# Kernel tuning notes

Hardware: AMD Instinct MI355X
Metric: run time of the kernel (lower is better)

The kernel has to match this reference:

```python
import jax, jax.numpy as jnp
import numpy as np

N_NODES = 50000
N_EDGES = 800000
HIDDEN = 128
MLP_DIM = 64

def setup_inputs() -> dict:
    key = jax.random.key(0)
    k1, k2, k3, k4 = jax.random.split(key, 4)
    node_emb = jax.random.normal(k1, (N_NODES, HIDDEN), dtype=jnp.float32)
    edge_index = jax.random.randint(k2, (2, N_EDGES), 0, N_NODES, dtype=jnp.int64)
    # Xavier-uniform init like the torch module
    lim1 = float(np.sqrt(6.0 / (2 * HIDDEN + MLP_DIM)))
    lim2 = float(np.sqrt(6.0 / (MLP_DIM + 1)))
    W1 = jax.random.uniform(k3, (2 * HIDDEN, MLP_DIM), minval=-lim1, maxval=lim1, dtype=jnp.float32)
    b1 = jnp.zeros((MLP_DIM,), dtype=jnp.float32)
    W2 = jax.random.uniform(k4, (MLP_DIM, 1), minval=-lim2, maxval=lim2, dtype=jnp.float32)
    b2 = jnp.zeros((1,), dtype=jnp.float32)
    return {"node_emb": node_emb, "edge_index": edge_index, "W1": W1, "b1": b1, "W2": W2, "b2": b2}

def reference(node_emb, edge_index, W1, b1, W2, b2):
    src, dst = edge_index[0], edge_index[1]
    emb_src = node_emb[src]                      # [E, H] gather
    emb_dst = node_emb[dst]                      # [E, H] gather
    edge_emb = jnp.concatenate([emb_src, emb_dst], axis=1)  # [E, 2H]
    h = jax.nn.relu(edge_emb @ W1 + b1)          # [E, MLP_DIM]
    edge_logits = h @ W2 + b2                    # [E, 1]
    return edge_logits
```

## Files before the change

kernel.cpp:

```cpp
#include <hip/hip_runtime.h>


#define HIDDEN 128

typedef __attribute__((ext_vector_type(8))) short bf16x8;
typedef __attribute__((ext_vector_type(4))) float f32x4;
typedef __attribute__((ext_vector_type(8))) _Float16 half8;

__device__ inline unsigned short f32_to_bf16(float f) {
    unsigned int u = __float_as_uint(f);
    unsigned int r = (u + 0x7fffu + ((u >> 16) & 1u)) >> 16;
    return (unsigned short)r;
}

__global__ __launch_bounds__(256) void precompute_pq_mfma(
    const float* __restrict__ node_emb,
    const float* __restrict__ W1,
    _Float16* __restrict__ PQ,
    int n_nodes)
{
    __shared__ unsigned short As[128 * 136];
    __shared__ unsigned short Bt[128 * 136];

    const int t = threadIdx.x;
    const int m0 = blockIdx.x * 128;

    #pragma unroll 4
    for (int s = 0; s < 16; ++s) {
        int slot = s * 256 + t;
        int row = slot >> 5;
        int k0 = (slot & 31) * 4;
        int m = m0 + row;
        float4 v = make_float4(0.f, 0.f, 0.f, 0.f);
        if (m < n_nodes) v = *(const float4*)&node_emb[(size_t)m * 128 + k0];
        ushort4 w;
        w.x = f32_to_bf16(v.x); w.y = f32_to_bf16(v.y);
        w.z = f32_to_bf16(v.z); w.w = f32_to_bf16(v.w);
        *(ushort4*)&As[row * 136 + k0] = w;
    }
    for (int u = t; u < 256 * 64; u += 256) {
        int r = u >> 6;
        int c = u & 63;
        int j = (r < 128) ? c : (c + 64);
        int k = r & 127;
        Bt[j * 136 + k] = f32_to_bf16(W1[u]);
    }
    __syncthreads();

    const int wave = t >> 6;
    const int lane = t & 63;
    const int lrow = lane & 15;
    const int kq = (lane >> 4) * 8;

    f32x4 acc[2][8];
    #pragma unroll
    for (int rs = 0; rs < 2; ++rs)
        #pragma unroll
        for (int c = 0; c < 8; ++c)
            acc[rs][c] = (f32x4){0.f, 0.f, 0.f, 0.f};

    #pragma unroll
    for (int k0 = 0; k0 < 128; k0 += 32) {
        bf16x8 a[2];
        #pragma unroll
        for (int rs = 0; rs < 2; ++rs)
            a[rs] = *(const bf16x8*)&As[(wave * 32 + rs * 16 + lrow) * 136 + k0 + kq];
        #pragma unroll
        for (int c = 0; c < 8; ++c) {
            bf16x8 b = *(const bf16x8*)&Bt[(c * 16 + lrow) * 136 + k0 + kq];
            acc[0][c] = __builtin_amdgcn_mfma_f32_16x16x32_bf16(a[0], b, acc[0][c], 0, 0, 0);
            acc[1][c] = __builtin_amdgcn_mfma_f32_16x16x32_bf16(a[1], b, acc[1][c], 0, 0, 0);
        }
    }

    const int rbase = (lane >> 4) * 4;
    #pragma unroll
    for (int rs = 0; rs < 2; ++rs) {
        #pragma unroll
        for (int reg = 0; reg < 4; ++reg) {
            int m = m0 + wave * 32 + rs * 16 + rbase + reg;
            if (m < n_nodes) {
                #pragma unroll
                for (int c = 0; c < 8; ++c) {
                    int col = c * 16 + lrow;
                    PQ[(size_t)m * 128 + col] = (_Float16)acc[rs][c][reg];
                }
            }
        }
    }
}

__global__ __launch_bounds__(256) void edge_mlp16(
    const _Float16* __restrict__ PQ,
    const int* __restrict__ edge_index,
    const float* __restrict__ b1,
    const float* __restrict__ W2,
    const float* __restrict__ b2,
    float* __restrict__ out,
    int E)
{
    const int t = threadIdx.x;
    const int g = t & 7;
    const int e = blockIdx.x * 32 + (t >> 3);
    if (e >= E) return;

    const int src = edge_index[e];
    const int dst = edge_index[E + e];

    half8 p = *(const half8*)&PQ[(size_t)src * 128 + g * 8];
    half8 q = *(const half8*)&PQ[(size_t)dst * 128 + 64 + g * 8];
    float4 bA = *(const float4*)&b1[g * 8];
    float4 bB = *(const float4*)&b1[g * 8 + 4];
    float4 wA = *(const float4*)&W2[g * 8];
    float4 wB = *(const float4*)&W2[g * 8 + 4];

    float partial = 0.f;
    partial += fmaxf((float)p[0] + (float)q[0] + bA.x, 0.f) * wA.x;
    partial += fmaxf((float)p[1] + (float)q[1] + bA.y, 0.f) * wA.y;
    partial += fmaxf((float)p[2] + (float)q[2] + bA.z, 0.f) * wA.z;
    partial += fmaxf((float)p[3] + (float)q[3] + bA.w, 0.f) * wA.w;
    partial += fmaxf((float)p[4] + (float)q[4] + bB.x, 0.f) * wB.x;
    partial += fmaxf((float)p[5] + (float)q[5] + bB.y, 0.f) * wB.y;
    partial += fmaxf((float)p[6] + (float)q[6] + bB.z, 0.f) * wB.z;
    partial += fmaxf((float)p[7] + (float)q[7] + bB.w, 0.f) * wB.w;

    partial += __shfl_xor(partial, 1, 64);
    partial += __shfl_xor(partial, 2, 64);
    partial += __shfl_xor(partial, 4, 64);

    if (g == 0) out[e] = partial + b2[0];
}

extern "C" void kernel_launch(void* const* d_in, const int* in_sizes, int n_in,
                              void* d_out, int out_size, void* d_ws, size_t ws_size,
                              hipStream_t stream) {
    const float* node_emb   = (const float*)d_in[0];
    const int*   edge_index = (const int*)d_in[1];
    const float* W1 = (const float*)d_in[2];
    const float* b1 = (const float*)d_in[3];
    const float* W2 = (const float*)d_in[4];
    const float* b2 = (const float*)d_in[5];
    float* out = (float*)d_out;

    const int n_nodes = in_sizes[0] / HIDDEN;
    const int E = in_sizes[1] / 2;

    _Float16* PQ = (_Float16*)d_ws;

    const int grid1 = (n_nodes + 127) / 128;
    precompute_pq_mfma<<<grid1, 256, 0, stream>>>(node_emb, W1, PQ, n_nodes);

    const int grid2 = (E + 31) / 32;
    edge_mlp16<<<grid2, 256, 0, stream>>>(PQ, edge_index, b1, W2, b2, out, E);
}
```

Measured before the change: 120.2 us.

## Fold b1 into node precompute, stage PQ stores via LDS, two edges per thread

The node precompute kernel now loads its A fragments straight from global memory into registers instead of staging them through LDS. It works on 64-node tiles, adds b1 into the P half, and writes PQ through an LDS buffer so global stores are coalesced 16-byte writes. The edge kernel handles two edges per 8-lane group so more gathers are in flight, and no longer loads b1. Smaller precompute tiles mean more blocks and more redundant W1 transposes, and the A loads from global are strided per lane.

After: 115.2 us. -4.2%, faster.

```diff
diff --git a/kernel.cpp b/kernel.cpp
--- a/kernel.cpp
+++ b/kernel.cpp
@@ -1,4 +1,5 @@
 #include <hip/hip_runtime.h>
+#include <hip/hip_bf16.h>
 
 
 #define HIDDEN 128
@@ -13,87 +14,99 @@
     return (unsigned short)r;
 }
 
-__global__ __launch_bounds__(256) void precompute_pq_mfma(
+__global__ __launch_bounds__(256, 2) void precompute_pq_mfma(
     const float* __restrict__ node_emb,
     const float* __restrict__ W1,
+    const float* __restrict__ b1,
     _Float16* __restrict__ PQ,
     int n_nodes)
 {
-    __shared__ unsigned short As[128 * 136];
     __shared__ unsigned short Bt[128 * 136];
+    __shared__ _Float16 Out[64 * 136];
 
     const int t = threadIdx.x;
-    const int m0 = blockIdx.x * 128;
+    const int wave = t >> 6, lane = t & 63;
+    const int lrow = lane & 15;
+    const int kq = (lane >> 4) * 8;
+    const int m0 = blockIdx.x * 64;
+    const int m = m0 + wave * 16 + lrow;
+    const bool valid = (m < n_nodes);
 
-    #pragma unroll 4
-    for (int s = 0; s < 16; ++s) {
-        int slot = s * 256 + t;
-        int row = slot >> 5;
-        int k0 = (slot & 31) * 4;
-        int m = m0 + row;
-        float4 v = make_float4(0.f, 0.f, 0.f, 0.f);
-        if (m < n_nodes) v = *(const float4*)&node_emb[(size_t)m * 128 + k0];
-        ushort4 w;
-        w.x = f32_to_bf16(v.x); w.y = f32_to_bf16(v.y);
-        w.z = f32_to_bf16(v.z); w.w = f32_to_bf16(v.w);
-        *(ushort4*)&As[row * 136 + k0] = w;
+    const float* arow = node_emb + (size_t)(valid ? m : 0) * HIDDEN + kq;
+    float4 aLo[4], aHi[4];
+    #pragma unroll
+    for (int i = 0; i < 4; ++i) {
+        if (valid) {
+            aLo[i] = *(const float4*)(arow + i * 32);
+            aHi[i] = *(const float4*)(arow + i * 32 + 4);
+        } else {
+            aLo[i] = make_float4(0.f, 0.f, 0.f, 0.f);
+            aHi[i] = aLo[i];
+        }
     }
-    for (int u = t; u < 256 * 64; u += 256) {
-        int r = u >> 6;
-        int c = u & 63;
-        int j = (r < 128) ? c : (c + 64);
+
+    #pragma unroll
+    for (int it = 0; it < 16; ++it) {
+        int slot = it * 256 + t;
+        int r = slot >> 4;
+        int c4 = (slot & 15) * 4;
+        float4 v = *(const float4*)&W1[r * 64 + c4];
+        int j = (r < 128) ? c4 : (c4 + 64);
         int k = r & 127;
-        Bt[j * 136 + k] = f32_to_bf16(W1[u]);
+        Bt[(j + 0) * 136 + k] = f32_to_bf16(v.x);
+        Bt[(j + 1) * 136 + k] = f32_to_bf16(v.y);
+        Bt[(j + 2) * 136 + k] = f32_to_bf16(v.z);
+        Bt[(j + 3) * 136 + k] = f32_to_bf16(v.w);
     }
     __syncthreads();
 
-    const int wave = t >> 6;
-    const int lane = t & 63;
-    const int lrow = lane & 15;
-    const int kq = (lane >> 4) * 8;
-
-    f32x4 acc[2][8];
+    f32x4 acc[8];
     #pragma unroll
-    for (int rs = 0; rs < 2; ++rs)
-        #pragma unroll
-        for (int c = 0; c < 8; ++c)
-            acc[rs][c] = (f32x4){0.f, 0.f, 0.f, 0.f};
+    for (int c = 0; c < 8; ++c) acc[c] = (f32x4){0.f, 0.f, 0.f, 0.f};
 
     #pragma unroll
-    for (int k0 = 0; k0 < 128; k0 += 32) {
-        bf16x8 a[2];
-        #pragma unroll
-        for (int rs = 0; rs < 2; ++rs)
-            a[rs] = *(const bf16x8*)&As[(wave * 32 + rs * 16 + lrow) * 136 + k0 + kq];
+    for (int k0i = 0; k0i < 4; ++k0i) {
+        union { bf16x8 v; __hip_bfloat162 h[4]; } ua;
+        ua.h[0] = __float22bfloat162_rn(make_float2(aLo[k0i].x, aLo[k0i].y));
+        ua.h[1] = __float22bfloat162_rn(make_float2(aLo[k0i].z, aLo[k0i].w));
+        ua.h[2] = __float22bfloat162_rn(make_float2(aHi[k0i].x, aHi[k0i].y));
+        ua.h[3] = __float22bfloat162_rn(make_float2(aHi[k0i].z, aHi[k0i].w));
+        const int kbase = k0i * 32 + kq;
         #pragma unroll
         for (int c = 0; c < 8; ++c) {
-            bf16x8 b = *(const bf16x8*)&Bt[(c * 16 + lrow) * 136 + k0 + kq];
-            acc[0][c] = __builtin_amdgcn_mfma_f32_16x16x32_bf16(a[0], b, acc[0][c], 0, 0, 0);
-            acc[1][c] = __builtin_amdgcn_mfma_f32_16x16x32_bf16(a[1], b, acc[1][c], 0, 0, 0);
+            bf16x8 bf = *(const bf16x8*)&Bt[(c * 16 + lrow) * 136 + kbase];
+            acc[c] = __builtin_amdgcn_mfma_f32_16x16x32_bf16(ua.v, bf, acc[c], 0, 0, 0);
         }
     }
 
     const int rbase = (lane >> 4) * 4;
     #pragma unroll
-    for (int rs = 0; rs < 2; ++rs) {
+    for (int c = 0; c < 8; ++c) {
+        int col = c * 16 + lrow;
+        float bias = (col < 64) ? b1[col] : 0.f;
         #pragma unroll
         for (int reg = 0; reg < 4; ++reg) {
-            int m = m0 + wave * 32 + rs * 16 + rbase + reg;
-            if (m < n_nodes) {
-                #pragma unroll
-                for (int c = 0; c < 8; ++c) {
-                    int col = c * 16 + lrow;
-                    PQ[(size_t)m * 128 + col] = (_Float16)acc[rs][c][reg];
-                }
-            }
+            int row = wave * 16 + rbase + reg;
+            Out[row * 136 + col] = (_Float16)(acc[c][reg] + bias);
+        }
+    }
+    __syncthreads();
+    #pragma unroll
+    for (int i = 0; i < 4; ++i) {
+        int idx = i * 256 + t;
+        int row = idx >> 4;
+        int cg = (idx & 15) * 8;
+        int mm = m0 + row;
+        if (mm < n_nodes) {
+            half8 v = *(const half8*)&Out[row * 136 + cg];
+            *(half8*)&PQ[(size_t)mm * HIDDEN + cg] = v;
         }
     }
 }
 
-__global__ __launch_bounds__(256) void edge_mlp16(
+__global__ __launch_bounds__(256, 4) void edge_mlp16(
     const _Float16* __restrict__ PQ,
     const int* __restrict__ edge_index,
-    const float* __restrict__ b1,
     const float* __restrict__ W2,
     const float* __restrict__ b2,
     float* __restrict__ out,
@@ -101,34 +114,56 @@
 {
     const int t = threadIdx.x;
     const int g = t & 7;
-    const int e = blockIdx.x * 32 + (t >> 3);
-    if (e >= E) return;
+    const int slot = t >> 3;
+    const int e0 = blockIdx.x * 64 + slot;
+    const int e1 = e0 + 32;
 
-    const int src = edge_index[e];
-    const int dst = edge_index[E + e];
-
-    half8 p = *(const half8*)&PQ[(size_t)src * 128 + g * 8];
-    half8 q = *(const half8*)&PQ[(size_t)dst * 128 + 64 + g * 8];
-    float4 bA = *(const float4*)&b1[g * 8];
-    float4 bB = *(const float4*)&b1[g * 8 + 4];
     float4 wA = *(const float4*)&W2[g * 8];
     float4 wB = *(const float4*)&W2[g * 8 + 4];
 
-    float partial = 0.f;
-    partial += fmaxf((float)p[0] + (float)q[0] + bA.x, 0.f) * wA.x;
-    partial += fmaxf((float)p[1] + (float)q[1] + bA.y, 0.f) * wA.y;
-    partial += fmaxf((float)p[2] + (float)q[2] + bA.z, 0.f) * wA.z;
-    partial += fmaxf((float)p[3] + (float)q[3] + bA.w, 0.f) * wA.w;
-    partial += fmaxf((float)p[4] + (float)q[4] + bB.x, 0.f) * wB.x;
-    partial += fmaxf((float)p[5] + (float)q[5] + bB.y, 0.f) * wB.y;
-    partial += fmaxf((float)p[6] + (float)q[6] + bB.z, 0.f) * wB.z;
-    partial += fmaxf((float)p[7] + (float)q[7] + bB.w, 0.f) * wB.w;
+    const bool v0 = e0 < E, v1 = e1 < E;
+    int src0 = 0, dst0 = 0, src1 = 0, dst1 = 0;
+    if (v0) { src0 = edge_index[e0]; dst0 = edge_index[E + e0]; }
+    if (v1) { src1 = edge_index[e1]; dst1 = edge_index[E + e1]; }
 
-    partial += __shfl_xor(partial, 1, 64);
-    partial += __shfl_xor(partial, 2, 64);
-    partial += __shfl_xor(partial, 4, 64);
+    half8 p0{}, q0{}, p1{}, q1{};
+    if (v0) {
+        p0 = *(const half8*)&PQ[(size_t)src0 * HIDDEN + g * 8];
+        q0 = *(const half8*)&PQ[(size_t)dst0 * HIDDEN + 64 + g * 8];
+    }
+    if (v1) {
+        p1 = *(const half8*)&PQ[(size_t)src1 * HIDDEN + g * 8];
+        q1 = *(const half8*)&PQ[(size_t)dst1 * HIDDEN + 64 + g * 8];
+    }
 
-    if (g == 0) out[e] = partial + b2[0];
+    float s0 = 0.f, s1 = 0.f;
+    s0 += fmaxf((float)p0[0] + (float)q0[0], 0.f) * wA.x;
+    s0 += fmaxf((float)p0[1] + (float)q0[1], 0.f) * wA.y;
+    s0 += fmaxf((float)p0[2] + (float)q0[2], 0.f) * wA.z;
+    s0 += fmaxf((float)p0[3] + (float)q0[3], 0.f) * wA.w;
+    s0 += fmaxf((float)p0[4] + (float)q0[4], 0.f) * wB.x;
+    s0 += fmaxf((float)p0[5] + (float)q0[5], 0.f) * wB.y;
+    s0 += fmaxf((float)p0[6] + (float)q0[6], 0.f) * wB.z;
+    s0 += fmaxf((float)p0[7] + (float)q0[7], 0.f) * wB.w;
+
+    s1 += fmaxf((float)p1[0] + (float)q1[0], 0.f) * wA.x;
+    s1 += fmaxf((float)p1[1] + (float)q1[1], 0.f) * wA.y;
+    s1 += fmaxf((float)p1[2] + (float)q1[2], 0.f) * wA.z;
+    s1 += fmaxf((float)p1[3] + (float)q1[3], 0.f) * wA.w;
+    s1 += fmaxf((float)p1[4] + (float)q1[4], 0.f) * wB.x;
+    s1 += fmaxf((float)p1[5] + (float)q1[5], 0.f) * wB.y;
+    s1 += fmaxf((float)p1[6] + (float)q1[6], 0.f) * wB.z;
+    s1 += fmaxf((float)p1[7] + (float)q1[7], 0.f) * wB.w;
+
+    s0 += __shfl_xor(s0, 1, 64);  s1 += __shfl_xor(s1, 1, 64);
+    s0 += __shfl_xor(s0, 2, 64);  s1 += __shfl_xor(s1, 2, 64);
+    s0 += __shfl_xor(s0, 4, 64);  s1 += __shfl_xor(s1, 4, 64);
+
+    if (g == 0) {
+        float bb = b2[0];
+        if (v0) out[e0] = s0 + bb;
+        if (v1) out[e1] = s1 + bb;
+    }
 }
 
 extern "C" void kernel_launch(void* const* d_in, const int* in_sizes, int n_in,
@@ -147,9 +182,9 @@
 
     _Float16* PQ = (_Float16*)d_ws;
 
-    const int grid1 = (n_nodes + 127) / 128;
-    precompute_pq_mfma<<<grid1, 256, 0, stream>>>(node_emb, W1, PQ, n_nodes);
+    const int grid1 = (n_nodes + 63) / 64;
+    precompute_pq_mfma<<<grid1, 256, 0, stream>>>(node_emb, W1, b1, PQ, n_nodes);
 
-    const int grid2 = (E + 31) / 32;
-    edge_mlp16<<<grid2, 256, 0, stream>>>(PQ, edge_index, b1, W2, b2, out, E);
+    const int grid2 = (E + 63) / 64;
+    edge_mlp16<<<grid2, 256, 0, stream>>>(PQ, edge_index, W2, b2, out, E);
 }
```
